# Optimization experiments

Hardware: AMD Instinct MI355X
Metric: run time of the kernel (lower is better)

The kernel has to match this reference:

```python
import jax, jax.numpy as jnp
import numpy as np

NUM_AGENTS = 5
B = 512          # graphs in batch
NP = 50          # nodes per graph
N = B * NP
EPG = 400        # edges per graph
E = B * EPG
H, C = 8, 64     # heads, per-head channels
F = H * C        # 512 node feature dim after concat
GRU_IN = 2 * F   # agent emb + graph emb
GRU_H = 128


def _gat_layer(x, src, dst, ea, W, a_src, a_dst, We, ae, b):
    # PyG GATConv: per-edge additive attention with edge features, softmax over dst
    n = x.shape[0]
    h = (x @ W).reshape(n, H, C)                          # [n,H,C]
    al = (h * a_src).sum(-1)[src] + (h * a_dst).sum(-1)[dst] \
         + ((ea @ We).reshape(-1, H, C) * ae).sum(-1)     # [e,H]
    al = jax.nn.leaky_relu(al, 0.2)
    amax = jax.ops.segment_max(al, dst, num_segments=n)
    amax = jnp.where(jnp.isfinite(amax), amax, 0.0)
    p = jnp.exp(al - amax[dst])
    denom = jax.ops.segment_sum(p, dst, num_segments=n)
    alpha = p / (denom[dst] + 1e-16)
    out = jax.ops.segment_sum(alpha[:, :, None] * h[src], dst, num_segments=n)
    return out.reshape(n, F) + b


def _gru(x_seq, h0, Wih, Whh, bih, bhh):
    # torch nn.GRU math, batch_first input [B,T,I]
    def step(h, x_t):
        gi = x_t @ Wih + bih
        gh = h @ Whh + bhh
        ir, iz, inn = jnp.split(gi, 3, axis=-1)
        hr, hz, hn = jnp.split(gh, 3, axis=-1)
        r = jax.nn.sigmoid(ir + hr)
        z = jax.nn.sigmoid(iz + hz)
        n_ = jnp.tanh(inn + r * hn)
        h_new = (1.0 - z) * n_ + z * h
        return h_new, h_new
    h_last, ys = jax.lax.scan(step, h0, jnp.swapaxes(x_seq, 0, 1))
    return jnp.swapaxes(ys, 0, 1), h_last


def _forward(x, edge_index, edge_attr, hidden_state,
             W1, a_src1, a_dst1, We1, ae1, b1,
             W2, a_src2, a_dst2, We2, ae2, b2,
             W3, a_src3, a_dst3, We3, ae3, b3,
             gru_Wih, gru_Whh, gru_bih, gru_bhh,
             fc1_W, fc1_b, fc2_W, fc2_b, log_std):
    src, dst = edge_index[0], edge_index[1]
    # conv1: add_self_loops=False
    x1 = jax.nn.relu(_gat_layer(x, src, dst, edge_attr, W1, a_src1, a_dst1, We1, ae1, b1))
    # conv2/3: add self loops with fill_value='mean' (mean of incoming edge_attr per node)
    cnt = jax.ops.segment_sum(jnp.ones((E,), x.dtype), dst, num_segments=N)
    loop_attr = jax.ops.segment_sum(edge_attr, dst, num_segments=N) / jnp.maximum(cnt, 1.0)[:, None]
    loops = jnp.arange(N, dtype=edge_index.dtype)
    src2 = jnp.concatenate([src, loops])
    dst2 = jnp.concatenate([dst, loops])
    ea2 = jnp.concatenate([edge_attr, loop_attr], axis=0)
    x2 = jax.nn.relu(_gat_layer(x1, src2, dst2, ea2, W2, a_src2, a_dst2, We2, ae2, b2))
    x3 = jax.nn.relu(_gat_layer(x2, src2, dst2, ea2, W3, a_src3, a_dst3, We3, ae3, b3))
    # global mean pool (each graph has NP nodes, contiguous)
    batch = jnp.repeat(jnp.arange(B), NP)
    graph_emb = jax.ops.segment_sum(x3, batch, num_segments=B) / NP   # [B,F]
    # first NUM_AGENTS nodes of each graph
    agent_idx = (jnp.arange(B)[:, None] * NP + jnp.arange(NUM_AGENTS)).reshape(-1)
    agent_emb = x3[agent_idx]                                          # [B*A,F]
    graph_rep = jnp.repeat(graph_emb, NUM_AGENTS, axis=0)
    combined = jnp.concatenate([agent_emb, graph_rep], axis=1).reshape(B, NUM_AGENTS, GRU_IN)
    gru_out, h_last = _gru(combined, hidden_state[0], gru_Wih, gru_Whh, gru_bih, gru_bhh)
    f1 = jax.nn.relu(gru_out.reshape(-1, GRU_H) @ fc1_W + fc1_b)
    action_mean = (f1 @ fc2_W + fc2_b).reshape(B, NUM_AGENTS, -1)
    action_std = jnp.broadcast_to(jnp.exp(jnp.clip(log_std, -20.0, 2.0)), action_mean.shape)
    return action_mean, action_std, h_last[None]


def setup_inputs() -> dict:
    ks = jax.random.split(jax.random.key(0), 24)
    rng = np.random.default_rng(0)
    # random edges within each graph, no self-loops
    src_l = rng.integers(0, NP, size=(B, EPG))
    dst_l = (src_l + 1 + rng.integers(0, NP - 1, size=(B, EPG))) % NP
    off = (np.arange(B) * NP)[:, None]
    edge_index = jnp.asarray(np.stack([(src_l + off).reshape(-1), (dst_l + off).reshape(-1)]), dtype=jnp.int32)

    def p(k, shape, fan):
        return jax.random.normal(k, shape, jnp.float32) / float(np.sqrt(fan))

    z = lambda *s: jnp.zeros(s, jnp.float32)
    return {
        "x": jax.random.normal(ks[0], (N, 4), jnp.float32),
        "edge_index": edge_index,
        "edge_attr": jax.random.uniform(ks[1], (E, 1), jnp.float32),
        "hidden_state": z(1, B, GRU_H),
        "W1": p(ks[2], (4, F), 4), "a_src1": p(ks[3], (H, C), C), "a_dst1": p(ks[4], (H, C), C),
        "We1": p(ks[5], (1, F), 1), "ae1": p(ks[6], (H, C), C), "b1": z(F),
        "W2": p(ks[7], (F, F), F), "a_src2": p(ks[8], (H, C), C), "a_dst2": p(ks[9], (H, C), C),
        "We2": p(ks[10], (1, F), 1), "ae2": p(ks[11], (H, C), C), "b2": z(F),
        "W3": p(ks[12], (F, F), F), "a_src3": p(ks[13], (H, C), C), "a_dst3": p(ks[14], (H, C), C),
        "We3": p(ks[15], (1, F), 1), "ae3": p(ks[16], (H, C), C), "b3": z(F),
        "gru_Wih": p(ks[17], (GRU_IN, 3 * GRU_H), GRU_IN),
        "gru_Whh": p(ks[18], (GRU_H, 3 * GRU_H), GRU_H),
        "gru_bih": z(3 * GRU_H), "gru_bhh": z(3 * GRU_H),
        "fc1_W": p(ks[19], (GRU_H, 64), GRU_H), "fc1_b": z(64),
        "fc2_W": p(ks[20], (64, 3), 64), "fc2_b": z(3),
        "log_std": jnp.full((1, 1, 3), -1.6, jnp.float32),
    }


def reference(x, edge_index, edge_attr, hidden_state,
              W1, a_src1, a_dst1, We1, ae1, b1,
              W2, a_src2, a_dst2, We2, ae2, b2,
              W3, a_src3, a_dst3, We3, ae3, b3,
              gru_Wih, gru_Whh, gru_bih, gru_bhh,
              fc1_W, fc1_b, fc2_W, fc2_b, log_std):
    return _forward(x, edge_index, edge_attr, hidden_state,
                    W1, a_src1, a_dst1, We1, ae1, b1,
                    W2, a_src2, a_dst2, We2, ae2, b2,
                    W3, a_src3, a_dst3, We3, ae3, b3,
                    gru_Wih, gru_Whh, gru_bih, gru_bhh,
                    fc1_W, fc1_b, fc2_W, fc2_b, log_std)
```

## Files before the change

### kernel.cpp

```cpp
#include <hip/hip_runtime.h>
#include <math.h>

#define NN 25600
#define BB 512
#define NP 50
#define EPG 400
#define EE 204800
#define HH 8
#define FF 512
#define GRUH 128
#define GRUIN 1024

typedef unsigned short ushort_t;
typedef __attribute__((ext_vector_type(8))) short bf16x8;
typedef __attribute__((ext_vector_type(4))) float f32x4;

__device__ __forceinline__ float wave_reduce_sum(float v) {
  #pragma unroll
  for (int m = 32; m >= 1; m >>= 1) v += __shfl_xor(v, m, 64);
  return v;
}

__device__ __forceinline__ ushort_t f2bf(float x) {
  union { float f; unsigned int u; } v; v.f = x;
  unsigned int r = v.u + 0x7fffu + ((v.u >> 16) & 1u);
  return (ushort_t)(r >> 16);
}

__device__ __forceinline__ float bf2f(ushort_t u) {
  union { unsigned int u; float f; } v; v.u = ((unsigned int)u) << 16;
  return v.f;
}

__device__ __forceinline__ void gload_lds16(const ushort_t* g, ushort_t* l) {
  __builtin_amdgcn_global_load_lds(
      (const __attribute__((address_space(1))) void*)g,
      (__attribute__((address_space(3))) void*)l, 16, 0, 0);
}

__global__ __launch_bounds__(256) void k_pre(
    const float* __restrict__ W2, const float* __restrict__ W3,
    const float* __restrict__ Wih,
    ushort_t* __restrict__ w2t, ushort_t* __restrict__ w3t, ushort_t* __restrict__ wiht,
    const int* __restrict__ ei, const float* __restrict__ eattr,
    int* __restrict__ rowp, ushort_t* __restrict__ esrc, float* __restrict__ eea,
    float* __restrict__ lattr,
    const float* __restrict__ We1, const float* __restrict__ ae1,
    const float* __restrict__ We2, const float* __restrict__ ae2,
    const float* __restrict__ We3, const float* __restrict__ ae3,
    float* __restrict__ wdot) {
  int b = blockIdx.x, tid = threadIdx.x;
  __shared__ float t[32][33];
  __shared__ int cnt[NP];
  __shared__ float esum[NP];
  __shared__ int rp[NP + 1];
  __shared__ int cur[NP];

  if (b < 896) {
    const float* W; ushort_t* Wt; int K, N, n0, k0;
    if (b < 256)      { W = W2;  Wt = w2t;  K = 512;  N = 512; n0 = (b & 15) * 32;        k0 = (b >> 4) * 32; }
    else if (b < 512) { W = W3;  Wt = w3t;  K = 512;  N = 512; n0 = ((b - 256) & 15) * 32; k0 = ((b - 256) >> 4) * 32; }
    else              { W = Wih; Wt = wiht; K = 1024; N = 384; n0 = ((b - 512) % 12) * 32; k0 = ((b - 512) / 12) * 32; }
    int tx = tid & 31, ty = tid >> 5;
    #pragma unroll
    for (int i = 0; i < 4; i++)
      t[ty + i * 8][tx] = W[(size_t)(k0 + ty + i * 8) * N + n0 + tx];
    __syncthreads();
    #pragma unroll
    for (int i = 0; i < 4; i++)
      Wt[(size_t)(n0 + ty + i * 8) * K + k0 + tx] = f2bf(t[tx][ty + i * 8]);
  } else if (b < 1408) {
    int g = b - 896;
    if (tid < NP) { cnt[tid] = 0; esum[tid] = 0.f; }
    __syncthreads();
    for (int e = tid; e < EPG; e += 256) {
      int ge = g * EPG + e;
      int dl = ei[EE + ge] - g * NP;
      atomicAdd(&cnt[dl], 1);
      atomicAdd(&esum[dl], eattr[ge]);
    }
    __syncthreads();
    if (tid == 0) {
      int s = 0;
      for (int i = 0; i < NP; i++) { rp[i] = s; cur[i] = s; s += cnt[i]; }
      rp[NP] = s;
    }
    __syncthreads();
    if (tid <= NP) rowp[g * 64 + tid] = rp[tid];
    if (tid < NP) lattr[g * NP + tid] = esum[tid] / (float)max(cnt[tid], 1);
    for (int e = tid; e < EPG; e += 256) {
      int ge = g * EPG + e;
      int sl = ei[ge] - g * NP;
      int dl = ei[EE + ge] - g * NP;
      int pos = atomicAdd(&cur[dl], 1);
      esrc[g * EPG + pos] = (ushort_t)sl;
      eea[g * EPG + pos] = eattr[ge];
    }
  } else {
    int w = tid >> 6, lane = tid & 63;
    for (int i = 0; i < 6; i++) {
      int idx = w + 4 * i;
      int l = idx >> 3, h = idx & 7;
      const float* We = l == 0 ? We1 : (l == 1 ? We2 : We3);
      const float* ae = l == 0 ? ae1 : (l == 1 ? ae2 : ae3);
      float v = wave_reduce_sum(We[h * 64 + lane] * ae[h * 64 + lane]);
      if (lane == 0) wdot[l * 8 + h] = v;
    }
  }
}

__global__ __launch_bounds__(512, 4) void k_layer(
    const ushort_t* __restrict__ Xbf,
    const float* __restrict__ x4, const float* __restrict__ W1,
    const ushort_t* __restrict__ Wt,
    const float* __restrict__ a_src, const float* __restrict__ a_dst,
    ushort_t* __restrict__ xout, ushort_t* __restrict__ cbf,
    const int* __restrict__ rowp, const ushort_t* __restrict__ esrc,
    const float* __restrict__ eea, const float* __restrict__ lattr,
    const float* __restrict__ wdot_all, const float* __restrict__ bias,
    int layer, int self_loops) {
  int g = blockIdx.x, half = blockIdx.y, tid = threadIdx.x;
  int w = tid >> 6, l = tid & 63;
  int head = w & 3;
  int flb = head * 64 + (w >> 2) * 32;
  int fbase = half * 256;
  int m_l = l & 15, quad = l >> 4, rq = quad * 4, kq8 = quad * 8;

  __shared__ __align__(16) ushort_t hS[256 * 72];
  __shared__ __align__(16) ushort_t AmU[12800];
  __shared__ float pds[512], pdd[512];
  __shared__ float sslS[256], sdlS[256];
  __shared__ ushort_t esrcS[400];
  __shared__ float eeaS[400];
  __shared__ int rowpS[51];
  __shared__ float lattrS[50];

  for (int i = tid; i < 400; i += 512) { esrcS[i] = esrc[g * EPG + i]; eeaS[i] = eea[g * EPG + i]; }
  if (tid <= NP) rowpS[tid] = rowp[g * 64 + tid];
  if (tid < NP) lattrS[tid] = lattr[g * NP + tid];

  f32x4 acc[2][4];
  #pragma unroll
  for (int i = 0; i < 2; i++)
    #pragma unroll
    for (int j = 0; j < 4; j++) acc[i][j] = (f32x4){0.f, 0.f, 0.f, 0.f};

  if (layer == 0) {
    float* W1s = (float*)AmU;
    float* xs = (float*)AmU + 1024;
    for (int i = tid; i < 1024; i += 512)
      W1s[i] = W1[(i >> 8) * 512 + fbase + (i & 255)];
    if (tid < NP) *(float4*)(&xs[tid * 4]) = *(const float4*)(&x4[(size_t)(g * NP + tid) * 4]);
    else if (tid < 64) *(float4*)(&xs[tid * 4]) = make_float4(0.f, 0.f, 0.f, 0.f);
    __syncthreads();
    float xr[4][4];
    #pragma unroll
    for (int nt = 0; nt < 4; nt++)
      #pragma unroll
      for (int k = 0; k < 4; k++) xr[nt][k] = xs[(nt * 16 + m_l) * 4 + k];
    #pragma unroll
    for (int mt = 0; mt < 2; mt++) {
      float wv[4][4];
      #pragma unroll
      for (int r = 0; r < 4; r++)
        #pragma unroll
        for (int k = 0; k < 4; k++) wv[r][k] = W1s[k * 256 + flb + mt * 16 + rq + r];
      #pragma unroll
      for (int nt = 0; nt < 4; nt++)
        #pragma unroll
        for (int r = 0; r < 4; r++)
          acc[mt][nt][r] = xr[nt][0] * wv[r][0] + xr[nt][1] * wv[r][1]
                         + xr[nt][2] * wv[r][2] + xr[nt][3] * wv[r][3];
    }
    __syncthreads();
  } else {
    ushort_t* hA = hS;
    ushort_t* hB = AmU;
    int arow = (l >> 3), acol = (l & 7) * 8;
    for (int k0 = 0; k0 < FF; k0 += 64) {
      #pragma unroll
      for (int j = 0; j < 4; j++)
        gload_lds16(Wt + (size_t)(fbase + w * 32 + j * 8 + arow) * FF + k0 + acol,
                    hA + w * 2048 + j * 512);
      gload_lds16(Xbf + (size_t)(g * NP + w * 8 + arow) * FF + k0 + acol,
                  hB + w * 512);
      __syncthreads();
      #pragma unroll
      for (int kc = 0; kc < 2; kc++) {
        bf16x8 bfr[4];
        #pragma unroll
        for (int nt = 0; nt < 4; nt++)
          bfr[nt] = *(const bf16x8*)(hB + (nt * 16 + m_l) * 64 + kc * 32 + kq8);
        #pragma unroll
        for (int mt = 0; mt < 2; mt++) {
          bf16x8 af = *(const bf16x8*)(hA + (flb + mt * 16 + m_l) * 64 + kc * 32 + kq8);
          #pragma unroll
          for (int nt = 0; nt < 4; nt++)
            acc[mt][nt] = __builtin_amdgcn_mfma_f32_16x16x32_bf16(af, bfr[nt], acc[mt][nt], 0, 0, 0);
        }
      }
      __syncthreads();
    }
  }

  float ds[4] = {0.f, 0.f, 0.f, 0.f}, dd[4] = {0.f, 0.f, 0.f, 0.f};
  int rbase = (m_l & 1) * 2;
  #pragma unroll
  for (int mt = 0; mt < 2; mt++) {
    float a_s[4], a_d[4];
    #pragma unroll
    for (int r = 0; r < 4; r++) {
      int fg = fbase + flb + mt * 16 + rq + r;
      a_s[r] = a_src[fg]; a_d[r] = a_dst[fg];
    }
    #pragma unroll
    for (int nt = 0; nt < 4; nt++) {
      unsigned int pk[4];
      #pragma unroll
      for (int r = 0; r < 4; r++) {
        float v = acc[mt][nt][r];
        ds[nt] += v * a_s[r];
        dd[nt] += v * a_d[r];
        float o = __shfl_xor(v, 1, 64);
        unsigned int own = f2bf(v), oth = f2bf(o);
        pk[r] = (m_l & 1) ? (oth | (own << 16)) : (own | (oth << 16));
      }
      int col = nt * 16 + (m_l & ~1);
      int row0 = flb + mt * 16 + rq + rbase;
      *(unsigned int*)(&hS[row0 * 72 + col]) = pk[rbase];
      *(unsigned int*)(&hS[(row0 + 1) * 72 + col]) = pk[rbase + 1];
    }
  }
  #pragma unroll
  for (int nt = 0; nt < 4; nt++) {
    ds[nt] += __shfl_xor(ds[nt], 16, 64); ds[nt] += __shfl_xor(ds[nt], 32, 64);
    dd[nt] += __shfl_xor(dd[nt], 16, 64); dd[nt] += __shfl_xor(dd[nt], 32, 64);
  }
  if (l < 16) {
    #pragma unroll
    for (int nt = 0; nt < 4; nt++) {
      pds[w * 64 + nt * 16 + l] = ds[nt];
      pdd[w * 64 + nt * 16 + l] = dd[nt];
    }
  }
  __syncthreads();

  { uint4* z = (uint4*)AmU; for (int i = tid; i < 1600; i += 512) z[i] = make_uint4(0u, 0u, 0u, 0u); }
  if (tid < 256) {
    sslS[tid] = pds[tid] + pds[tid + 256];
    sdlS[tid] = pdd[tid] + pdd[tid + 256];
  }
  __syncthreads();

  float wdot = wdot_all[layer * 8 + half * 4 + head];
  if (w < 4 && l < NP) {
    ushort_t* AmH = AmU + w * 3200;
    int d = l;
    int e0 = rowpS[d], e1 = rowpS[d + 1];
    float sd = sdlS[w * 64 + d];
    float m = -1e30f;
    for (int e = e0; e < e1; e++) {
      float al = sslS[w * 64 + esrcS[e]] + sd + eeaS[e] * wdot;
      al = al > 0.f ? al : 0.2f * al;
      m = fmaxf(m, al);
    }
    float al_loop = 0.f;
    if (self_loops) {
      al_loop = sslS[w * 64 + d] + sd + lattrS[d] * wdot;
      al_loop = al_loop > 0.f ? al_loop : 0.2f * al_loop;
      m = fmaxf(m, al_loop);
    }
    if (e1 > e0 || self_loops) {
      float denom = 0.f;
      for (int e = e0; e < e1; e++) {
        float al = sslS[w * 64 + esrcS[e]] + sd + eeaS[e] * wdot;
        al = al > 0.f ? al : 0.2f * al;
        float p = __expf(al - m);
        denom += p;
        int sp = esrcS[e] ^ ((d & 3) << 3);
        float prev = bf2f(AmH[d * 64 + sp]);
        AmH[d * 64 + sp] = f2bf(prev + p);
      }
      if (self_loops) {
        float p = __expf(al_loop - m);
        denom += p;
        int sp = d ^ ((d & 3) << 3);
        float prev = bf2f(AmH[d * 64 + sp]);
        AmH[d * 64 + sp] = f2bf(prev + p);
      }
      float inv = 1.f / (denom + 1e-16f);
      #pragma unroll
      for (int c = 0; c < 8; c++) {
        union { ushort_t u[8]; uint4 q; } pk;
        pk.q = *(uint4*)(AmH + d * 64 + c * 8);
        #pragma unroll
        for (int j = 0; j < 8; j++) pk.u[j] = f2bf(bf2f(pk.u[j]) * inv);
        *(uint4*)(AmH + d * 64 + c * 8) = pk.q;
      }
    }
  }
  __syncthreads();

  ushort_t* AmW = AmU + head * 3200;
  f32x4 oacc[2][4];
  #pragma unroll
  for (int i = 0; i < 2; i++)
    #pragma unroll
    for (int j = 0; j < 4; j++) oacc[i][j] = (f32x4){0.f, 0.f, 0.f, 0.f};
  #pragma unroll
  for (int kc = 0; kc < 2; kc++) {
    int kb = kc * 32 + kq8;
    bf16x8 bfr2[4];
    #pragma unroll
    for (int nt = 0; nt < 4; nt++) {
      int d = nt * 16 + m_l;
      int rd = d < NP ? d : 0;
      bfr2[nt] = *(const bf16x8*)(AmW + rd * 64 + (kb ^ ((rd & 3) << 3)));
    }
    #pragma unroll
    for (int mt = 0; mt < 2; mt++) {
      int fl = flb + mt * 16 + m_l;
      bf16x8 afr = *(const bf16x8*)(&hS[fl * 72 + kb]);
      #pragma unroll
      for (int nt = 0; nt < 4; nt++)
        oacc[mt][nt] = __builtin_amdgcn_mfma_f32_16x16x32_bf16(afr, bfr2[nt], oacc[mt][nt], 0, 0, 0);
    }
  }

  float vv[2][4][4];
  #pragma unroll
  for (int mt = 0; mt < 2; mt++) {
    const float4 bv = *(const float4*)(&bias[fbase + flb + mt * 16 + rq]);
    #pragma unroll
    for (int nt = 0; nt < 4; nt++) {
      vv[mt][nt][0] = fmaxf(oacc[mt][nt][0] + bv.x, 0.f);
      vv[mt][nt][1] = fmaxf(oacc[mt][nt][1] + bv.y, 0.f);
      vv[mt][nt][2] = fmaxf(oacc[mt][nt][2] + bv.z, 0.f);
      vv[mt][nt][3] = fmaxf(oacc[mt][nt][3] + bv.w, 0.f);
    }
  }

  if (cbf == nullptr) {
    #pragma unroll
    for (int nt = 0; nt < 4; nt++) {
      int d = nt * 16 + m_l;
      if (d < NP) {
        #pragma unroll
        for (int mt = 0; mt < 2; mt++) {
          union { ushort_t u[4]; uint2 v; } pk;
          #pragma unroll
          for (int r = 0; r < 4; r++) pk.u[r] = f2bf(vv[mt][nt][r]);
          *(uint2*)(&xout[(size_t)(g * NP + d) * FF + fbase + flb + mt * 16 + rq]) = pk.v;
        }
      }
    }
  } else {
    #pragma unroll
    for (int mt = 0; mt < 2; mt++) {
      float msum[4];
      #pragma unroll
      for (int r = 0; r < 4; r++) {
        float t = 0.f;
        #pragma unroll
        for (int nt = 0; nt < 4; nt++) {
          int d = nt * 16 + m_l;
          t += (d < NP) ? vv[mt][nt][r] : 0.f;
        }
        t += __shfl_xor(t, 1, 64); t += __shfl_xor(t, 2, 64);
        t += __shfl_xor(t, 4, 64); t += __shfl_xor(t, 8, 64);
        msum[r] = t * (1.f / NP);
      }
      if (m_l == 0) {
        union { ushort_t u[4]; uint2 v; } pk;
        #pragma unroll
        for (int r = 0; r < 4; r++) pk.u[r] = f2bf(msum[r]);
        #pragma unroll
        for (int t5 = 0; t5 < 5; t5++)
          *(uint2*)(&cbf[(size_t)(g * 5 + t5) * GRUIN + 512 + fbase + flb + mt * 16 + rq]) = pk.v;
      }
      if (m_l < 5) {
        union { ushort_t u[4]; uint2 v; } pk;
        #pragma unroll
        for (int r = 0; r < 4; r++) pk.u[r] = f2bf(vv[mt][0][r]);
        *(uint2*)(&cbf[(size_t)(g * 5 + m_l) * GRUIN + fbase + flb + mt * 16 + rq]) = pk.v;
      }
    }
  }
}

__global__ __launch_bounds__(256) void k_bgemm(
    const ushort_t* __restrict__ A, const ushort_t* __restrict__ Bt,
    const float* __restrict__ bias, float* __restrict__ C,
    int M, int N, int K) {
  __shared__ ushort_t As[128 * 32];
  __shared__ ushort_t Bs[128 * 32];
  int tid = threadIdx.x;
  int w = tid >> 6, l = tid & 63;
  int row0 = blockIdx.y * 128, col0 = blockIdx.x * 128;
  int wr = w >> 1, wc = w & 1;

  f32x4 acc[4][4];
  #pragma unroll
  for (int i = 0; i < 4; i++)
    #pragma unroll
    for (int j = 0; j < 4; j++) acc[i][j] = (f32x4){0.f, 0.f, 0.f, 0.f};

  int srow = w * 32 + (l >> 2);
  int skcol = (l & 3) * 8;
  const ushort_t* Ag = A + (size_t)(row0 + srow) * K + skcol;
  const ushort_t* Bg = Bt + (size_t)(col0 + srow) * K + skcol;
  ushort_t* AsW = &As[w * 1024];
  ushort_t* BsW = &Bs[w * 1024];

  int m_l = l & 15, kq = (l >> 4) * 8;
  const ushort_t* ArdA = &As[(wr * 64 + m_l) * 32 + kq];
  const ushort_t* BrdB = &Bs[(wc * 64 + m_l) * 32 + kq];

  for (int k0 = 0; k0 < K; k0 += 32) {
    gload_lds16(Ag + k0, AsW);
    gload_lds16(Ag + (size_t)16 * K + k0, AsW + 512);
    gload_lds16(Bg + k0, BsW);
    gload_lds16(Bg + (size_t)16 * K + k0, BsW + 512);
    __syncthreads();
    bf16x8 af[4], bfr[4];
    #pragma unroll
    for (int t = 0; t < 4; t++) {
      af[t]  = *(const bf16x8*)(ArdA + t * 16 * 32);
      bfr[t] = *(const bf16x8*)(BrdB + t * 16 * 32);
    }
    #pragma unroll
    for (int mt = 0; mt < 4; mt++)
      #pragma unroll
      for (int nt = 0; nt < 4; nt++)
        acc[mt][nt] = __builtin_amdgcn_mfma_f32_16x16x32_bf16(af[mt], bfr[nt], acc[mt][nt], 0, 0, 0);
    __syncthreads();
  }

  int cl = l & 15, rq = (l >> 4) * 4;
  #pragma unroll
  for (int mt = 0; mt < 4; mt++) {
    #pragma unroll
    for (int nt = 0; nt < 4; nt++) {
      int col = col0 + wc * 64 + nt * 16 + cl;
      float bv = bias ? bias[col] : 0.f;
      #pragma unroll
      for (int r = 0; r < 4; r++) {
        int row = row0 + wr * 64 + mt * 16 + rq + r;
        C[(size_t)row * N + col] = acc[mt][nt][r] + bv;
      }
    }
  }
}

__global__ void k_grufc(const float* __restrict__ gi_all, const float* __restrict__ h0,
                        const float* __restrict__ Whh, const float* __restrict__ bhh,
                        const float* __restrict__ fc1W, const float* __restrict__ fc1b,
                        const float* __restrict__ fc2W, const float* __restrict__ fc2b,
                        const float* __restrict__ log_std, float* __restrict__ dout) {
  int b = blockIdx.x, tid = threadIdx.x;
  __shared__ float hl[GRUH];
  __shared__ float ghb[384];
  __shared__ float go[5 * GRUH];
  __shared__ float f1[5 * 64];
  if (tid < GRUH) hl[tid] = h0[b * GRUH + tid];
  for (int t = 0; t < 5; t++) {
    __syncthreads();
    float acc = bhh[tid];
    for (int k = 0; k < GRUH; k++) acc += hl[k] * Whh[k * 384 + tid];
    ghb[tid] = acc;
    __syncthreads();
    if (tid < GRUH) {
      const float* gi = gi_all + (size_t)(b * 5 + t) * 384;
      float r = 1.f / (1.f + expf(-(gi[tid] + ghb[tid])));
      float z = 1.f / (1.f + expf(-(gi[128 + tid] + ghb[128 + tid])));
      float nn = tanhf(gi[256 + tid] + r * ghb[256 + tid]);
      float hn = (1.f - z) * nn + z * hl[tid];
      go[t * GRUH + tid] = hn;
      hl[tid] = hn;
    }
  }
  __syncthreads();
  if (tid < GRUH) dout[15360 + b * GRUH + tid] = hl[tid];
  if (tid < 320) {
    int t = tid >> 6, j = tid & 63;
    float acc = fc1b[j];
    for (int k = 0; k < GRUH; k++) acc += go[t * GRUH + k] * fc1W[k * 64 + j];
    f1[t * 64 + j] = fmaxf(acc, 0.f);
  }
  __syncthreads();
  if (tid < 15) {
    int t = tid / 3, o = tid % 3;
    float v = fc2b[o];
    for (int j = 0; j < 64; j++) v += f1[t * 64 + j] * fc2W[j * 3 + o];
    dout[(b * 5 + t) * 3 + o] = v;
    float ls = log_std[o];
    ls = fminf(fmaxf(ls, -20.f), 2.f);
    dout[7680 + (b * 5 + t) * 3 + o] = expf(ls);
  }
}

extern "C" void kernel_launch(void* const* d_in, const int* in_sizes, int n_in,
                              void* d_out, int out_size, void* d_ws, size_t ws_size,
                              hipStream_t stream) {
  const float* x      = (const float*)d_in[0];
  const int*   ei     = (const int*)d_in[1];
  const float* eattr  = (const float*)d_in[2];
  const float* hstate = (const float*)d_in[3];
  const float* W1  = (const float*)d_in[4];
  const float* as1 = (const float*)d_in[5];
  const float* ad1 = (const float*)d_in[6];
  const float* We1 = (const float*)d_in[7];
  const float* ae1 = (const float*)d_in[8];
  const float* b1  = (const float*)d_in[9];
  const float* W2  = (const float*)d_in[10];
  const float* as2 = (const float*)d_in[11];
  const float* ad2 = (const float*)d_in[12];
  const float* We2 = (const float*)d_in[13];
  const float* ae2 = (const float*)d_in[14];
  const float* b2  = (const float*)d_in[15];
  const float* W3  = (const float*)d_in[16];
  const float* as3 = (const float*)d_in[17];
  const float* ad3 = (const float*)d_in[18];
  const float* We3 = (const float*)d_in[19];
  const float* ae3 = (const float*)d_in[20];
  const float* b3  = (const float*)d_in[21];
  const float* Wih = (const float*)d_in[22];
  const float* Whh = (const float*)d_in[23];
  const float* bih = (const float*)d_in[24];
  const float* bhh = (const float*)d_in[25];
  const float* fc1W = (const float*)d_in[26];
  const float* fc1b = (const float*)d_in[27];
  const float* fc2W = (const float*)d_in[28];
  const float* fc2b = (const float*)d_in[29];
  const float* lstd = (const float*)d_in[30];

  float* ws = (float*)d_ws;
  ushort_t* xbf1 = (ushort_t*)ws;
  ushort_t* xbf2 = (ushort_t*)(ws + 6569984);
  float* p = ws + 2 * 6569984;
  int*   rowp  = (int*)p;         p += 32768;
  ushort_t* esrc = (ushort_t*)p;  p += 102400;
  float* eea   = p;               p += 204800;
  float* lattr = p;               p += 25600;
  float* wdot  = p;               p += 32;
  ushort_t* w2t  = (ushort_t*)p;  p += 131072;
  ushort_t* w3t  = (ushort_t*)p;  p += 131072;
  ushort_t* wiht = (ushort_t*)p;  p += 196608;
  ushort_t* cbf  = (ushort_t*)p;  p += 1310720;
  float* gi_all  = p;             p += 983040;
  float* dout = (float*)d_out;

  k_pre<<<1409, 256, 0, stream>>>(W2, W3, Wih, w2t, w3t, wiht, ei, eattr,
                                  rowp, esrc, eea, lattr,
                                  We1, ae1, We2, ae2, We3, ae3, wdot);

  k_layer<<<dim3(BB, 2), 512, 0, stream>>>(nullptr, x, W1, nullptr, as1, ad1,
                                           xbf1, nullptr, rowp, esrc, eea, lattr,
                                           wdot, b1, 0, 0);
  k_layer<<<dim3(BB, 2), 512, 0, stream>>>(xbf1, nullptr, nullptr, w2t, as2, ad2,
                                           xbf2, nullptr, rowp, esrc, eea, lattr,
                                           wdot, b2, 1, 1);
  k_layer<<<dim3(BB, 2), 512, 0, stream>>>(xbf2, nullptr, nullptr, w3t, as3, ad3,
                                           nullptr, cbf, rowp, esrc, eea, lattr,
                                           wdot, b3, 2, 1);

  k_bgemm<<<dim3(3, 20), 256, 0, stream>>>(cbf, wiht, bih, gi_all, 2560, 384, GRUIN);

  k_grufc<<<BB, 384, 0, stream>>>(gi_all, hstate, Whh, bhh, fc1W, fc1b,
                                  fc2W, fc2b, lstd, dout);
}
```

Baseline: 319.7 us.

## Split GAT layer blocks into quarters of features with 256 threads

Each k_layer block now covers 128 output features (two heads) with 256 threads instead of 256 features with 512 threads, so the grid doubles to BB x 4. The K-loop tile shrinks from 64 to 32, and the padded h tile in shared memory is replaced by an XOR-swizzled layout written per element. Each block uses less shared memory, which should fit more blocks per CU and raise occupancy. In exchange the per-graph edge and attention work is repeated across four blocks instead of two, and the X tile is reloaded more times.

Result: faster. 293.4 us (-8.2%).

```diff
diff --git a/kernel.cpp b/kernel.cpp
--- a/kernel.cpp
+++ b/kernel.cpp
@@ -109,7 +109,7 @@
   }
 }
 
-__global__ __launch_bounds__(512, 4) void k_layer(
+__global__ __launch_bounds__(256, 4) void k_layer(
     const ushort_t* __restrict__ Xbf,
     const float* __restrict__ x4, const float* __restrict__ W1,
     const ushort_t* __restrict__ Wt,
@@ -119,23 +119,22 @@
     const float* __restrict__ eea, const float* __restrict__ lattr,
     const float* __restrict__ wdot_all, const float* __restrict__ bias,
     int layer, int self_loops) {
-  int g = blockIdx.x, half = blockIdx.y, tid = threadIdx.x;
+  int g = blockIdx.x, q = blockIdx.y, tid = threadIdx.x;
   int w = tid >> 6, l = tid & 63;
-  int head = w & 3;
-  int flb = head * 64 + (w >> 2) * 32;
-  int fbase = half * 256;
+  int fbase = q * 128;
+  int head_local = w >> 1;
   int m_l = l & 15, quad = l >> 4, rq = quad * 4, kq8 = quad * 8;
 
-  __shared__ __align__(16) ushort_t hS[256 * 72];
-  __shared__ __align__(16) ushort_t AmU[12800];
-  __shared__ float pds[512], pdd[512];
-  __shared__ float sslS[256], sdlS[256];
+  __shared__ __align__(16) ushort_t hS[128 * 64];
+  __shared__ __align__(16) ushort_t AmU[6400];
+  __shared__ float pds[4 * 64], pdd[4 * 64];
+  __shared__ float sslS[128], sdlS[128];
   __shared__ ushort_t esrcS[400];
   __shared__ float eeaS[400];
   __shared__ int rowpS[51];
   __shared__ float lattrS[50];
 
-  for (int i = tid; i < 400; i += 512) { esrcS[i] = esrc[g * EPG + i]; eeaS[i] = eea[g * EPG + i]; }
+  for (int i = tid; i < 400; i += 256) { esrcS[i] = esrc[g * EPG + i]; eeaS[i] = eea[g * EPG + i]; }
   if (tid <= NP) rowpS[tid] = rowp[g * 64 + tid];
   if (tid < NP) lattrS[tid] = lattr[g * NP + tid];
 
@@ -147,9 +146,9 @@
 
   if (layer == 0) {
     float* W1s = (float*)AmU;
-    float* xs = (float*)AmU + 1024;
-    for (int i = tid; i < 1024; i += 512)
-      W1s[i] = W1[(i >> 8) * 512 + fbase + (i & 255)];
+    float* xs = (float*)AmU + 512;
+    for (int i = tid; i < 512; i += 256)
+      W1s[i] = W1[(i >> 7) * 512 + fbase + (i & 127)];
     if (tid < NP) *(float4*)(&xs[tid * 4]) = *(const float4*)(&x4[(size_t)(g * NP + tid) * 4]);
     else if (tid < 64) *(float4*)(&xs[tid * 4]) = make_float4(0.f, 0.f, 0.f, 0.f);
     __syncthreads();
@@ -164,7 +163,7 @@
       #pragma unroll
       for (int r = 0; r < 4; r++)
         #pragma unroll
-        for (int k = 0; k < 4; k++) wv[r][k] = W1s[k * 256 + flb + mt * 16 + rq + r];
+        for (int k = 0; k < 4; k++) wv[r][k] = W1s[k * 128 + w * 32 + mt * 16 + rq + r];
       #pragma unroll
       for (int nt = 0; nt < 4; nt++)
         #pragma unroll
@@ -174,61 +173,52 @@
     }
     __syncthreads();
   } else {
-    ushort_t* hA = hS;
-    ushort_t* hB = AmU;
-    int arow = (l >> 3), acol = (l & 7) * 8;
-    for (int k0 = 0; k0 < FF; k0 += 64) {
-      #pragma unroll
-      for (int j = 0; j < 4; j++)
-        gload_lds16(Wt + (size_t)(fbase + w * 32 + j * 8 + arow) * FF + k0 + acol,
-                    hA + w * 2048 + j * 512);
-      gload_lds16(Xbf + (size_t)(g * NP + w * 8 + arow) * FF + k0 + acol,
-                  hB + w * 512);
+    ushort_t* As = hS;
+    ushort_t* Bs = AmU;
+    const ushort_t* AgBase = Wt + (size_t)(fbase + w * 32 + (l >> 2)) * FF + (l & 3) * 8;
+    const ushort_t* Bg = Xbf + (size_t)(g * NP + w * 16 + (l >> 2)) * FF + (l & 3) * 8;
+    ushort_t* AsW = As + w * 1024;
+    ushort_t* BsW = Bs + w * 512;
+    for (int k0 = 0; k0 < FF; k0 += 32) {
+      gload_lds16(AgBase + k0, AsW);
+      gload_lds16(AgBase + (size_t)16 * FF + k0, AsW + 512);
+      gload_lds16(Bg + k0, BsW);
       __syncthreads();
-      #pragma unroll
-      for (int kc = 0; kc < 2; kc++) {
-        bf16x8 bfr[4];
+      bf16x8 bfr[4];
+      #pragma unroll
+      for (int nt = 0; nt < 4; nt++)
+        bfr[nt] = *(const bf16x8*)(Bs + (nt * 16 + m_l) * 32 + kq8);
+      #pragma unroll
+      for (int mt = 0; mt < 2; mt++) {
+        bf16x8 af = *(const bf16x8*)(As + (w * 32 + mt * 16 + m_l) * 32 + kq8);
         #pragma unroll
         for (int nt = 0; nt < 4; nt++)
-          bfr[nt] = *(const bf16x8*)(hB + (nt * 16 + m_l) * 64 + kc * 32 + kq8);
-        #pragma unroll
-        for (int mt = 0; mt < 2; mt++) {
-          bf16x8 af = *(const bf16x8*)(hA + (flb + mt * 16 + m_l) * 64 + kc * 32 + kq8);
-          #pragma unroll
-          for (int nt = 0; nt < 4; nt++)
-            acc[mt][nt] = __builtin_amdgcn_mfma_f32_16x16x32_bf16(af, bfr[nt], acc[mt][nt], 0, 0, 0);
-        }
+          acc[mt][nt] = __builtin_amdgcn_mfma_f32_16x16x32_bf16(af, bfr[nt], acc[mt][nt], 0, 0, 0);
       }
       __syncthreads();
     }
   }
 
   float ds[4] = {0.f, 0.f, 0.f, 0.f}, dd[4] = {0.f, 0.f, 0.f, 0.f};
-  int rbase = (m_l & 1) * 2;
   #pragma unroll
   for (int mt = 0; mt < 2; mt++) {
     float a_s[4], a_d[4];
     #pragma unroll
     for (int r = 0; r < 4; r++) {
-      int fg = fbase + flb + mt * 16 + rq + r;
+      int fg = fbase + w * 32 + mt * 16 + rq + r;
       a_s[r] = a_src[fg]; a_d[r] = a_dst[fg];
     }
     #pragma unroll
     for (int nt = 0; nt < 4; nt++) {
-      unsigned int pk[4];
+      int s = nt * 16 + m_l;
       #pragma unroll
       for (int r = 0; r < 4; r++) {
         float v = acc[mt][nt][r];
         ds[nt] += v * a_s[r];
         dd[nt] += v * a_d[r];
-        float o = __shfl_xor(v, 1, 64);
-        unsigned int own = f2bf(v), oth = f2bf(o);
-        pk[r] = (m_l & 1) ? (oth | (own << 16)) : (own | (oth << 16));
-      }
-      int col = nt * 16 + (m_l & ~1);
-      int row0 = flb + mt * 16 + rq + rbase;
-      *(unsigned int*)(&hS[row0 * 72 + col]) = pk[rbase];
-      *(unsigned int*)(&hS[(row0 + 1) * 72 + col]) = pk[rbase + 1];
+        int fl = w * 32 + mt * 16 + rq + r;
+        hS[fl * 64 + (s ^ ((fl & 3) << 3))] = f2bf(v);
+      }
     }
   }
   #pragma unroll
@@ -245,15 +235,16 @@
   }
   __syncthreads();
 
-  { uint4* z = (uint4*)AmU; for (int i = tid; i < 1600; i += 512) z[i] = make_uint4(0u, 0u, 0u, 0u); }
-  if (tid < 256) {
-    sslS[tid] = pds[tid] + pds[tid + 256];
-    sdlS[tid] = pdd[tid] + pdd[tid + 256];
+  { uint4* z = (uint4*)AmU; for (int i = tid; i < 800; i += 256) z[i] = make_uint4(0u, 0u, 0u, 0u); }
+  if (tid < 128) {
+    int base = (tid >> 6) * 128 + (tid & 63);
+    sslS[tid] = pds[base] + pds[base + 64];
+    sdlS[tid] = pdd[base] + pdd[base + 64];
   }
   __syncthreads();
 
-  float wdot = wdot_all[layer * 8 + half * 4 + head];
-  if (w < 4 && l < NP) {
+  if (w < 2 && l < NP) {
+    float wdot = wdot_all[layer * 8 + q * 2 + w];
     ushort_t* AmH = AmU + w * 3200;
     int d = l;
     int e0 = rowpS[d], e1 = rowpS[d + 1];
@@ -291,17 +282,17 @@
       float inv = 1.f / (denom + 1e-16f);
       #pragma unroll
       for (int c = 0; c < 8; c++) {
-        union { ushort_t u[8]; uint4 q; } pk;
-        pk.q = *(uint4*)(AmH + d * 64 + c * 8);
+        union { ushort_t u[8]; uint4 q2; } pk;
+        pk.q2 = *(uint4*)(AmH + d * 64 + c * 8);
         #pragma unroll
         for (int j = 0; j < 8; j++) pk.u[j] = f2bf(bf2f(pk.u[j]) * inv);
-        *(uint4*)(AmH + d * 64 + c * 8) = pk.q;
+        *(uint4*)(AmH + d * 64 + c * 8) = pk.q2;
       }
     }
   }
   __syncthreads();
 
-  ushort_t* AmW = AmU + head * 3200;
+  ushort_t* AmW = AmU + head_local * 3200;
   f32x4 oacc[2][4];
   #pragma unroll
   for (int i = 0; i < 2; i++)
@@ -319,8 +310,8 @@
     }
     #pragma unroll
     for (int mt = 0; mt < 2; mt++) {
-      int fl = flb + mt * 16 + m_l;
-      bf16x8 afr = *(const bf16x8*)(&hS[fl * 72 + kb]);
+      int fl = w * 32 + mt * 16 + m_l;
+      bf16x8 afr = *(const bf16x8*)(hS + fl * 64 + (kb ^ ((fl & 3) << 3)));
       #pragma unroll
       for (int nt = 0; nt < 4; nt++)
         oacc[mt][nt] = __builtin_amdgcn_mfma_f32_16x16x32_bf16(afr, bfr2[nt], oacc[mt][nt], 0, 0, 0);
@@ -330,7 +321,7 @@
   float vv[2][4][4];
   #pragma unroll
   for (int mt = 0; mt < 2; mt++) {
-    const float4 bv = *(const float4*)(&bias[fbase + flb + mt * 16 + rq]);
+    const float4 bv = *(const float4*)(&bias[fbase + w * 32 + mt * 16 + rq]);
     #pragma unroll
     for (int nt = 0; nt < 4; nt++) {
       vv[mt][nt][0] = fmaxf(oacc[mt][nt][0] + bv.x, 0.f);
@@ -350,7 +341,7 @@
           union { ushort_t u[4]; uint2 v; } pk;
           #pragma unroll
           for (int r = 0; r < 4; r++) pk.u[r] = f2bf(vv[mt][nt][r]);
-          *(uint2*)(&xout[(size_t)(g * NP + d) * FF + fbase + flb + mt * 16 + rq]) = pk.v;
+          *(uint2*)(&xout[(size_t)(g * NP + d) * FF + fbase + w * 32 + mt * 16 + rq]) = pk.v;
         }
       }
     }
@@ -376,13 +367,13 @@
         for (int r = 0; r < 4; r++) pk.u[r] = f2bf(msum[r]);
         #pragma unroll
         for (int t5 = 0; t5 < 5; t5++)
-          *(uint2*)(&cbf[(size_t)(g * 5 + t5) * GRUIN + 512 + fbase + flb + mt * 16 + rq]) = pk.v;
+          *(uint2*)(&cbf[(size_t)(g * 5 + t5) * GRUIN + 512 + fbase + w * 32 + mt * 16 + rq]) = pk.v;
       }
       if (m_l < 5) {
         union { ushort_t u[4]; uint2 v; } pk;
         #pragma unroll
         for (int r = 0; r < 4; r++) pk.u[r] = f2bf(vv[mt][0][r]);
-        *(uint2*)(&cbf[(size_t)(g * 5 + m_l) * GRUIN + fbase + flb + mt * 16 + rq]) = pk.v;
+        *(uint2*)(&cbf[(size_t)(g * 5 + m_l) * GRUIN + fbase + w * 32 + mt * 16 + rq]) = pk.v;
       }
     }
   }
@@ -554,13 +545,13 @@
                                   rowp, esrc, eea, lattr,
                                   We1, ae1, We2, ae2, We3, ae3, wdot);
 
-  k_layer<<<dim3(BB, 2), 512, 0, stream>>>(nullptr, x, W1, nullptr, as1, ad1,
+  k_layer<<<dim3(BB, 4), 256, 0, stream>>>(nullptr, x, W1, nullptr, as1, ad1,
                                            xbf1, nullptr, rowp, esrc, eea, lattr,
                                            wdot, b1, 0, 0);
-  k_layer<<<dim3(BB, 2), 512, 0, stream>>>(xbf1, nullptr, nullptr, w2t, as2, ad2,
+  k_layer<<<dim3(BB, 4), 256, 0, stream>>>(xbf1, nullptr, nullptr, w2t, as2, ad2,
                                            xbf2, nullptr, rowp, esrc, eea, lattr,
                                            wdot, b2, 1, 1);
-  k_layer<<<dim3(BB, 2), 512, 0, stream>>>(xbf2, nullptr, nullptr, w3t, as3, ad3,
+  k_layer<<<dim3(BB, 4), 256, 0, stream>>>(xbf2, nullptr, nullptr, w3t, as3, ad3,
                                            nullptr, cbf, rowp, esrc, eea, lattr,
                                            wdot, b3, 2, 1);
 
```
